# Performance work log

Hardware: AMD Instinct MI355X
Metric: run time of the kernel (lower is better)

Reference implementation:

```python
import jax, jax.numpy as jnp
import numpy as np


def setup_inputs() -> dict:
    key = jax.random.key(0)
    k1, k2, k3, k4 = jax.random.split(key, 4)
    B, N, F, S, OUT = 8, 50000, 32, 16, 64
    x = jax.random.normal(k1, (B, N, F), dtype=jnp.float32)
    spiral_adj = jax.random.randint(k2, (B, N, S), 0, N, dtype=jnp.int64)
    W = jax.random.normal(k3, (OUT, F * S), dtype=jnp.float32) * (1.0 / np.sqrt(F * S))
    b = jax.random.normal(k4, (OUT,), dtype=jnp.float32) * 0.01
    return {"x": x, "spiral_adj": spiral_adj, "W": W, "b": b}


def reference(x, spiral_adj, W, b):
    B, N, F = x.shape
    S = spiral_adj.shape[-1]
    # Per-batch gather of spiral neighbors: (B, N, S, F)
    spirals = jax.vmap(lambda xb, ab: xb[ab])(x, spiral_adj)
    spirals = spirals.reshape(B, N, S * F)
    # Linear: y = spirals @ W^T + b, then ELU
    out = jnp.einsum('bnk,ok->bno', spirals, W) + b
    out = jax.nn.elu(out)
    # zero out the last (padding) vertex
    mask = jnp.ones((1, N, 1), dtype=out.dtype).at[0, -1, 0].set(0.0)
    return out * mask
```

## Files before the change

kernel.cpp:

```cpp
#include <hip/hip_runtime.h>
#include <hip/hip_bf16.h>
#include <string.h>

#define B_ 8
#define N_ 50000
#define F_ 32
#define S_ 16
#define O_ 64
#define K_ (F_ * S_)
#define XELEMS (B_ * N_ * F_)
#define TPB (N_ / 16)
#define BPB 196

typedef __attribute__((ext_vector_type(8))) short bf16x8;
typedef __attribute__((ext_vector_type(4))) float f32x4;

union bfpack { bf16x8 v; __hip_bfloat16 h[8]; };

__global__ __launch_bounds__(256) void prep_kernel(const float* __restrict__ W,
                                                   unsigned short* __restrict__ Wb,
                                                   const float* __restrict__ x,
                                                   unsigned short* __restrict__ xb) {
    int bid = blockIdx.x;
    if (bid < 128) {
        int i = bid * 256 + threadIdx.x;
        int j = i & 7;
        int o = (i >> 3) & 63;
        int qk = i >> 9;
        int quad = qk & 3;
        int kt = qk >> 2;
        __hip_bfloat16 h = __float2bfloat16(W[o * K_ + kt * 32 + quad * 8 + j]);
        unsigned short u; memcpy(&u, &h, 2);
        Wb[i] = u;
    } else {
        int i = (bid - 128) * 256 + threadIdx.x;
        if (i < XELEMS / 8) {
            size_t base = (size_t)i * 8;
            f32x4 a = __builtin_nontemporal_load((const f32x4*)(x + base));
            f32x4 b = __builtin_nontemporal_load((const f32x4*)(x + base + 4));
            bfpack p;
            p.h[0] = __float2bfloat16(a[0]); p.h[1] = __float2bfloat16(a[1]);
            p.h[2] = __float2bfloat16(a[2]); p.h[3] = __float2bfloat16(a[3]);
            p.h[4] = __float2bfloat16(b[0]); p.h[5] = __float2bfloat16(b[1]);
            p.h[6] = __float2bfloat16(b[2]); p.h[7] = __float2bfloat16(b[3]);
            *(bf16x8*)(xb + base) = p.v;
        }
    }
}

__global__ __launch_bounds__(256) void spiral_kernel(
        const unsigned short* __restrict__ xb, const int* __restrict__ adj,
        const unsigned short* __restrict__ Wb, const float* __restrict__ bias,
        float* __restrict__ out) {
    const int lane = threadIdx.x & 63;
    const int wv   = threadIdx.x >> 6;
    const int m16  = lane & 15;
    const int quad = lane >> 4;

    const int b  = blockIdx.x & 7;
    const int jb = blockIdx.x >> 3;
    const int tib0 = (jb * 4 + wv) * 4;

    int rowbase[4];
    int nn[4];
#pragma unroll
    for (int vt = 0; vt < 4; ++vt) {
        int t = tib0 + vt;
        if (t >= TPB) t = TPB - 1;
        nn[vt] = t * 16;
        rowbase[vt] = b * N_ + t * 16;
    }
    const size_t xbase = (size_t)b * N_ * F_;

    f32x4 acc[4][4];
#pragma unroll
    for (int vt = 0; vt < 4; ++vt)
#pragma unroll
        for (int nt = 0; nt < 4; ++nt)
            acc[vt][nt] = (f32x4){0.f, 0.f, 0.f, 0.f};

#pragma unroll
    for (int kt4 = 0; kt4 < 4; ++kt4) {
        int4 aj[4];
#pragma unroll
        for (int vt = 0; vt < 4; ++vt)
            aj[vt] = *(const int4*)(adj + (size_t)(rowbase[vt] + m16) * S_ + kt4 * 4);

#pragma unroll
        for (int q = 0; q < 4; ++q) {
            const int kt = kt4 * 4 + q;
            bf16x8 xf[4];
#pragma unroll
            for (int vt = 0; vt < 4; ++vt) {
                int a = ((const int*)&aj[vt])[q];
                xf[vt] = *(const bf16x8*)(xb + xbase + (size_t)a * F_ + quad * 8);
            }
            bf16x8 wf[4];
#pragma unroll
            for (int nt = 0; nt < 4; ++nt)
                wf[nt] = *(const bf16x8*)(Wb + (size_t)((kt * 4 + quad) * 64 + nt * 16 + m16) * 8);
#pragma unroll
            for (int vt = 0; vt < 4; ++vt)
#pragma unroll
                for (int nt = 0; nt < 4; ++nt)
                    acc[vt][nt] = __builtin_amdgcn_mfma_f32_16x16x32_bf16(wf[nt], xf[vt], acc[vt][nt], 0, 0, 0);
        }
    }

#pragma unroll
    for (int vt = 0; vt < 4; ++vt) {
        const int n = nn[vt] + m16;
        const bool zero = (n == N_ - 1);
        float* orow = out + (size_t)(rowbase[vt] + m16) * O_ + quad * 4;
#pragma unroll
        for (int nt = 0; nt < 4; ++nt) {
            f32x4 bv = *(const f32x4*)(bias + nt * 16 + quad * 4);
            f32x4 v;
#pragma unroll
            for (int r = 0; r < 4; ++r) {
                float t = acc[vt][nt][r] + bv[r];
                t = t > 0.f ? t : (__expf(t) - 1.f);
                v[r] = zero ? 0.f : t;
            }
            *(f32x4*)(orow + nt * 16) = v;
        }
    }
}

__global__ __launch_bounds__(256) void wconv_kernel(const float* __restrict__ W,
                                                    unsigned short* __restrict__ Wb) {
    int i = blockIdx.x * 256 + threadIdx.x;
    if (i < O_ * K_) {
        int j = i & 7, o = (i >> 3) & 63, qk = i >> 9;
        int quad = qk & 3, kt = qk >> 2;
        __hip_bfloat16 h = __float2bfloat16(W[o * K_ + kt * 32 + quad * 8 + j]);
        unsigned short u; memcpy(&u, &h, 2);
        Wb[i] = u;
    }
}

__global__ __launch_bounds__(256) void spiral_f32_kernel(
        const float* __restrict__ x, const int* __restrict__ adj,
        const unsigned short* __restrict__ Wb, const float* __restrict__ bias,
        float* __restrict__ out) {
    const int lane = threadIdx.x & 63;
    const int wv = threadIdx.x >> 6;
    const int m16 = lane & 15, quad = lane >> 4;
    const int b  = blockIdx.x & 7;
    const int jb = blockIdx.x >> 3;
    const int tib0 = (jb * 4 + wv) * 4;
    int rowbase[4], nn[4];
#pragma unroll
    for (int vt = 0; vt < 4; ++vt) {
        int t = tib0 + vt;
        if (t >= TPB) t = TPB - 1;
        nn[vt] = t * 16;
        rowbase[vt] = b * N_ + t * 16;
    }
    f32x4 acc[4][4];
#pragma unroll
    for (int vt = 0; vt < 4; ++vt)
#pragma unroll
        for (int nt = 0; nt < 4; ++nt) acc[vt][nt] = (f32x4){0.f,0.f,0.f,0.f};
    for (int kt = 0; kt < 16; ++kt) {
        bf16x8 wf[4];
#pragma unroll
        for (int nt = 0; nt < 4; ++nt)
            wf[nt] = *(const bf16x8*)(Wb + (size_t)((kt * 4 + quad) * 64 + nt * 16 + m16) * 8);
#pragma unroll
        for (int vt = 0; vt < 4; ++vt) {
            int a = adj[(size_t)(rowbase[vt] + m16) * S_ + kt];
            const float* xr = x + ((size_t)b * N_ + a) * F_ + quad * 8;
            f32x4 x0 = *(const f32x4*)xr;
            f32x4 x1 = *(const f32x4*)(xr + 4);
            bfpack af;
            af.h[0]=__float2bfloat16(x0[0]); af.h[1]=__float2bfloat16(x0[1]);
            af.h[2]=__float2bfloat16(x0[2]); af.h[3]=__float2bfloat16(x0[3]);
            af.h[4]=__float2bfloat16(x1[0]); af.h[5]=__float2bfloat16(x1[1]);
            af.h[6]=__float2bfloat16(x1[2]); af.h[7]=__float2bfloat16(x1[3]);
#pragma unroll
            for (int nt = 0; nt < 4; ++nt)
                acc[vt][nt] = __builtin_amdgcn_mfma_f32_16x16x32_bf16(wf[nt], af.v, acc[vt][nt], 0, 0, 0);
        }
    }
#pragma unroll
    for (int vt = 0; vt < 4; ++vt) {
        const int n = nn[vt] + m16;
        const bool zero = (n == N_ - 1);
        float* orow = out + (size_t)(rowbase[vt] + m16) * O_ + quad * 4;
#pragma unroll
        for (int nt = 0; nt < 4; ++nt) {
            f32x4 bv = *(const f32x4*)(bias + nt * 16 + quad * 4);
            f32x4 v;
#pragma unroll
            for (int r = 0; r < 4; ++r) {
                float t = acc[vt][nt][r] + bv[r];
                t = t > 0.f ? t : (__expf(t) - 1.f);
                v[r] = zero ? 0.f : t;
            }
            *(f32x4*)(orow + nt * 16) = v;
        }
    }
}

extern "C" void kernel_launch(void* const* d_in, const int* in_sizes, int n_in,
                              void* d_out, int out_size, void* d_ws, size_t ws_size,
                              hipStream_t stream) {
    const float* x    = (const float*)d_in[0];
    const int*   adj  = (const int*)d_in[1];
    const float* W    = (const float*)d_in[2];
    const float* bias = (const float*)d_in[3];
    float* out = (float*)d_out;

    const size_t wb_bytes = (size_t)O_ * K_ * 2;
    const size_t xb_bytes = (size_t)XELEMS * 2;
    unsigned short* Wb = (unsigned short*)d_ws;
    unsigned short* xb = (unsigned short*)((char*)d_ws + wb_bytes);

    const int grid_main = 8 * BPB;

    if (ws_size >= wb_bytes + xb_bytes) {
        int grid_prep = 128 + (XELEMS / 8 + 255) / 256;
        hipLaunchKernelGGL(prep_kernel, dim3(grid_prep), dim3(256), 0, stream, W, Wb, x, xb);
        hipLaunchKernelGGL(spiral_kernel, dim3(grid_main), dim3(256), 0, stream,
                           xb, adj, Wb, bias, out);
    } else {
        hipLaunchKernelGGL(wconv_kernel, dim3(128), dim3(256), 0, stream, W, Wb);
        hipLaunchKernelGGL(spiral_f32_kernel, dim3(grid_main), dim3(256), 0, stream,
                           x, adj, Wb, bias, out);
    }
}
```

Baseline: 235.6 us.

## Pipeline spiral gathers through LDS ring with async global_load_lds prefetch

Loads all adjacency indices up front, then gathers the neighbor feature rows through a 4-deep per-wave LDS ring using global_load_lds. W fragments are prefetched three steps ahead into registers. Explicit vmcnt waits and sched barriers keep several gather steps in flight while the MFMAs run, which is meant to hide gather latency. The cost is 64KB of LDS per block, a min-blocks launch bound that caps registers, and hand-counted waitcnt values that break if the compiler emits a different number of memory ops.

```diff
diff --git a/kernel.cpp b/kernel.cpp
--- a/kernel.cpp
+++ b/kernel.cpp
@@ -14,6 +14,7 @@
 
 typedef __attribute__((ext_vector_type(8))) short bf16x8;
 typedef __attribute__((ext_vector_type(4))) float f32x4;
+typedef __attribute__((ext_vector_type(4))) int int4v;
 
 union bfpack { bf16x8 v; __hip_bfloat16 h[8]; };
 
@@ -48,7 +49,7 @@
     }
 }
 
-__global__ __launch_bounds__(256) void spiral_kernel(
+__global__ __launch_bounds__(256, 2) void spiral_kernel(
         const unsigned short* __restrict__ xb, const int* __restrict__ adj,
         const unsigned short* __restrict__ Wb, const float* __restrict__ bias,
         float* __restrict__ out) {
@@ -61,6 +62,8 @@
     const int jb = blockIdx.x >> 3;
     const int tib0 = (jb * 4 + wv) * 4;
 
+    __shared__ __align__(16) unsigned char ring[4][4][4][1024];
+
     int rowbase[4];
     int nn[4];
 #pragma unroll
@@ -72,6 +75,14 @@
     }
     const size_t xbase = (size_t)b * N_ * F_;
 
+    int4v aj_all[4][4];
+#pragma unroll
+    for (int vt = 0; vt < 4; ++vt)
+#pragma unroll
+        for (int kt4 = 0; kt4 < 4; ++kt4)
+            aj_all[vt][kt4] = __builtin_nontemporal_load(
+                (const int4v*)(adj + (size_t)(rowbase[vt] + m16) * S_ + kt4 * 4));
+
     f32x4 acc[4][4];
 #pragma unroll
     for (int vt = 0; vt < 4; ++vt)
@@ -79,33 +90,63 @@
         for (int nt = 0; nt < 4; ++nt)
             acc[vt][nt] = (f32x4){0.f, 0.f, 0.f, 0.f};
 
-#pragma unroll
-    for (int kt4 = 0; kt4 < 4; ++kt4) {
-        int4 aj[4];
+    bf16x8 wfp[4][4];
+
+#define GATHER_ISSUE(g_)                                                                   \
+    do {                                                                                   \
+        if ((g_) < 16) {                                                                   \
+            const int kt4_ = (g_) >> 2, q_ = (g_) & 3;                                     \
+            _Pragma("unroll")                                                              \
+            for (int vt = 0; vt < 4; ++vt) {                                               \
+                int a_ = aj_all[vt][kt4_][q_];                                             \
+                const unsigned short* src_ = xb + xbase + (size_t)a_ * F_ + quad * 8;      \
+                __builtin_amdgcn_global_load_lds(                                          \
+                    (const __attribute__((address_space(1))) void*)src_,                   \
+                    (__attribute__((address_space(3))) void*)&ring[wv][(g_) & 3][vt][0],   \
+                    16, 0, 0);                                                             \
+            }                                                                              \
+        }                                                                                  \
+    } while (0)
+
+#define LOAD_W(g_)                                                                         \
+    do {                                                                                   \
+        if ((g_) < 16) {                                                                   \
+            _Pragma("unroll")                                                              \
+            for (int nt = 0; nt < 4; ++nt)                                                 \
+                wfp[(g_) & 3][nt] = *(const bf16x8*)(                                      \
+                    Wb + (size_t)(((g_) * 4 + quad) * 64 + nt * 16 + m16) * 8);            \
+        }                                                                                  \
+    } while (0)
+
+#define SB __builtin_amdgcn_sched_barrier(0)
+
+    GATHER_ISSUE(0); SB; LOAD_W(0); SB;
+    GATHER_ISSUE(1); SB; LOAD_W(1); SB;
+    GATHER_ISSUE(2); SB; LOAD_W(2); SB;
+
+#pragma unroll
+    for (int g = 0; g < 16; ++g) {
+        GATHER_ISSUE(g + 3); SB;
+        LOAD_W(g + 3); SB;
+        if (g < 13)       asm volatile("s_waitcnt vmcnt(24)" ::: "memory");
+        else if (g == 13) asm volatile("s_waitcnt vmcnt(16)" ::: "memory");
+        else if (g == 14) asm volatile("s_waitcnt vmcnt(8)"  ::: "memory");
+        else              asm volatile("s_waitcnt vmcnt(0)"  ::: "memory");
+        SB;
+        bf16x8 xf[4];
 #pragma unroll
         for (int vt = 0; vt < 4; ++vt)
-            aj[vt] = *(const int4*)(adj + (size_t)(rowbase[vt] + m16) * S_ + kt4 * 4);
-
-#pragma unroll
-        for (int q = 0; q < 4; ++q) {
-            const int kt = kt4 * 4 + q;
-            bf16x8 xf[4];
-#pragma unroll
-            for (int vt = 0; vt < 4; ++vt) {
-                int a = ((const int*)&aj[vt])[q];
-                xf[vt] = *(const bf16x8*)(xb + xbase + (size_t)a * F_ + quad * 8);
-            }
-            bf16x8 wf[4];
+            xf[vt] = *(const bf16x8*)&ring[wv][g & 3][vt][(size_t)lane * 16];
+#pragma unroll
+        for (int vt = 0; vt < 4; ++vt)
 #pragma unroll
             for (int nt = 0; nt < 4; ++nt)
-                wf[nt] = *(const bf16x8*)(Wb + (size_t)((kt * 4 + quad) * 64 + nt * 16 + m16) * 8);
-#pragma unroll
-            for (int vt = 0; vt < 4; ++vt)
-#pragma unroll
-                for (int nt = 0; nt < 4; ++nt)
-                    acc[vt][nt] = __builtin_amdgcn_mfma_f32_16x16x32_bf16(wf[nt], xf[vt], acc[vt][nt], 0, 0, 0);
-        }
-    }
+                acc[vt][nt] = __builtin_amdgcn_mfma_f32_16x16x32_bf16(wfp[g & 3][nt], xf[vt], acc[vt][nt], 0, 0, 0);
+        SB;
+    }
+#undef GATHER_ISSUE
+#undef LOAD_W
+#undef SB
 
 #pragma unroll
     for (int vt = 0; vt < 4; ++vt) {
```

Result: faster. 230.5 us, median of 2 (-2.2%).
